# Optimization experiments

Measured on AMD Instinct MI355X. Metric: run time of the kernel, lower is better.

Reference implementation:

```python
import jax, jax.numpy as jnp
import numpy as np
from jax import lax

B, T, S, J, D = 8, 512, 32, 64, 400
R, MDU, TAGS = 256, 100, 7


def _lstm(x, Wih, Whh, bih, bhh):
    """PyTorch-convention LSTM over x [N,L,Din]; gate order i,f,g,o.
    Returns (hs, cs) each [N,L,R] in scan order (not re-flipped)."""
    N = x.shape[0]
    Rh = Whh.shape[1]
    h0 = jnp.zeros((N, Rh), x.dtype)
    xW = x @ Wih.T + (bih + bhh)  # precompute input projection [N,L,4R]

    def step(carry, xt):
        h, c = carry
        g = xt + h @ Whh.T
        i, f, gg, o = jnp.split(g, 4, axis=-1)
        c = jax.nn.sigmoid(f) * c + jax.nn.sigmoid(i) * jnp.tanh(gg)
        h = jax.nn.sigmoid(o) * jnp.tanh(c)
        return (h, c), (h, c)

    _, (hs, cs) = lax.scan(step, (h0, h0), xW.transpose(1, 0, 2))
    return hs.transpose(1, 0, 2), cs.transpose(1, 0, 2)


def setup_inputs() -> dict:
    key = jax.random.key(0)
    ks = jax.random.split(key, 40)

    def rn(i, shape, s=0.1):
        return s * jax.random.normal(ks[i], shape, jnp.float32)

    inp = {
        'input_text': rn(0, (B, T, D), 1.0),
        'input_syn': rn(1, (B, S, J, D), 1.0),
        'label': jax.random.randint(ks[2], (B, T), 0, TAGS),
        'len_context': jnp.full((B,), T, jnp.int32),
        'len_synopsis': jnp.full((B, S), J, jnp.int32),
    }
    # 6 LSTM parameter sets: context f1/b1 (in=D), synopsis f/b (in=D), modeling f/b (in=4R)
    idx = 3
    for name, din in [('f1', D), ('b1', D), ('sf', D), ('sb', D), ('mf', 4 * R), ('mb', 4 * R)]:
        inp['Wih_' + name] = rn(idx, (4 * R, din)); idx += 1
        inp['Whh_' + name] = rn(idx, (4 * R, R)); idx += 1
        inp['bih_' + name] = rn(idx, (4 * R,)); idx += 1
        inp['bhh_' + name] = rn(idx, (4 * R,)); idx += 1
    inp['W_cWh'] = rn(idx, (MDU, 2 * R)); idx += 1
    inp['W_cWu'] = rn(idx, (MDU, 2 * R)); idx += 1
    inp['W_v'] = rn(idx, (1, MDU)); idx += 1
    inp['W_sWh'] = rn(idx, (2 * R, 2 * R)); idx += 1
    inp['W_sWu'] = rn(idx, (2 * R, 2 * R)); idx += 1
    inp['W_Ws'] = rn(idx, (MDU, 2 * R)); idx += 1
    inp['W_out'] = rn(idx, (TAGS, 6 * R)); idx += 1
    inp['b_out'] = rn(idx, (TAGS,)); idx += 1
    return inp


def reference(input_text, input_syn, label, len_context, len_synopsis,
              Wih_f1, Whh_f1, bih_f1, bhh_f1,
              Wih_b1, Whh_b1, bih_b1, bhh_b1,
              Wih_sf, Whh_sf, bih_sf, bhh_sf,
              Wih_sb, Whh_sb, bih_sb, bhh_sb,
              Wih_mf, Whh_mf, bih_mf, bhh_mf,
              Wih_mb, Whh_mb, bih_mb, bhh_mb,
              W_cWh, W_cWu, W_v, W_sWh, W_sWu, W_Ws, W_out, b_out):
    B_, T_, D_ = input_text.shape
    S_, J_ = input_syn.shape[1], input_syn.shape[2]

    mask = (jnp.arange(T_)[None, :] < len_context[:, None]).astype(input_text.dtype)

    # --- representation layer: manual bi-LSTMCell; backward hiddens kept in scan order ---
    hs_f, cs_f = _lstm(input_text, Wih_f1, Whh_f1, bih_f1, bhh_f1)
    hs_b, cs_b = _lstm(input_text[:, ::-1], Wih_b1, Whh_b1, bih_b1, bhh_b1)
    H = jnp.concatenate([hs_f, hs_b], -1) * mask[..., None]   # [B,T,2R]
    m = jnp.concatenate([cs_f, cs_b], -1) * mask[..., None]   # [B,T,2R]
    x_init = jnp.zeros((B_, 1, 2 * R), input_text.dtype)
    H_full = jnp.concatenate([x_init, H], 1)                  # H_ : [B,T+1,2R]

    # --- synopsis encoder: bi-LSTM final hidden per synopsis sentence ---
    syn = input_syn.reshape(B_ * S_, J_, D_)
    sh_f, _ = _lstm(syn, Wih_sf, Whh_sf, bih_sf, bhh_sf)
    sh_b, _ = _lstm(syn[:, ::-1], Wih_sb, Whh_sb, bih_sb, bhh_sb)
    U = jnp.concatenate([sh_f[:, -1], sh_b[:, -1]], -1).reshape(B_, S_, 2 * R)

    # --- 'ff' co-attention ---
    cWh = H @ W_cWh.T                                          # [B,T,MDU]
    cWu = U @ W_cWu.T                                          # [B,S,MDU]
    z = jnp.tanh(cWh[:, :, None, :] + cWu[:, None, :, :]) @ W_v[0]  # [B,T,S]
    alpha = jax.nn.softmax(z, axis=-1)
    c = jnp.einsum('bts,bsd->btd', alpha, U)                   # [B,T,2R]

    # --- sentinel (ATT_SYN) ---
    Hprev = H_full[:, :T_]                                     # shifted: x_init, H[0..T-2]
    e = jax.nn.sigmoid(Hprev @ W_sWh.T + Hprev @ W_sWu.T)
    s = e * jnp.tanh(m)                                        # [B,T,2R]
    z_hat = jnp.tanh(s @ W_Ws.T + cWh) @ W_v[0]                # [B,T]
    alpha_hat = jax.nn.softmax(jnp.concatenate([z, z_hat[..., None]], -1), axis=-1)
    beta = alpha_hat[:, :, S_:S_ + 1]                          # [B,T,1]
    c_hat = beta * s + (1.0 - beta) * c
    G = jnp.concatenate([H, c_hat], -1)                        # [B,T,4R]

    # --- modeling bi-LSTM (standard aligned outputs) + output projection ---
    mh_f, _ = _lstm(G, Wih_mf, Whh_mf, bih_mf, bhh_mf)
    mh_b, _ = _lstm(G[:, ::-1], Wih_mb, Whh_mb, bih_mb, bhh_mb)
    M = jnp.concatenate([mh_f, mh_b[:, ::-1]], -1)             # [B,T,2R]

    logit = jnp.concatenate([G, M], -1) @ W_out.T + b_out      # [B,T,TAGS]
    return logit
```

## Files before the change

### kernel.cpp

```cpp
#include <hip/hip_runtime.h>
#include <math.h>
#include <stddef.h>


#define BB 8
#define TT 512
#define SS 32
#define JJ 64
#define DD 400
#define RR 256
#define G4 1024
#define H2 512
#define MDU_ 100
#define TAGS_ 7
#define BT (BB*TT)
#define NSEQ (BB*SS)
#define SCH 64
#define MB1 (1024*1024)

typedef __attribute__((ext_vector_type(8))) short short8;
typedef __attribute__((ext_vector_type(4))) float floatx4;
typedef __attribute__((ext_vector_type(4))) unsigned int u32x4;
typedef unsigned short u16;
typedef unsigned int u32;

__device__ __forceinline__ float us2f(u16 u) {
    unsigned int v = ((unsigned int)u) << 16;
    return __builtin_bit_cast(float, v);
}
__device__ __forceinline__ u16 f2us(float f) {
    unsigned int v = __builtin_bit_cast(unsigned int, f);
    v += 0x7FFFu + ((v >> 16) & 1u);
    return (u16)(v >> 16);
}
__device__ __forceinline__ float ldin(const void* p, long i, int bf) {
    return bf ? us2f(((const u16*)p)[i]) : ((const float*)p)[i];
}
__device__ __forceinline__ float sigm(float x) { return 1.0f / (1.0f + expf(-x)); }
__device__ __forceinline__ float sigm_f(float x) { return 1.0f / (1.0f + __expf(-x)); }
__device__ __forceinline__ float tanh_f(float x) {
    float e = __expf(-2.0f * fabsf(x));
    float t = (1.0f - e) / (1.0f + e);
    return copysignf(t, x);
}

__global__ void detect_k(const void* x, int* flag) {
    __shared__ int cnt;
    if (threadIdx.x == 0) cnt = 0;
    __syncthreads();
    u16 lo = ((const u16*)x)[threadIdx.x * 2];
    int e = (lo >> 7) & 0xFF;
    if (e >= 118 && e <= 131) atomicAdd(&cnt, 1);
    __syncthreads();
    if (threadIdx.x == 0) *flag = (cnt > 128) ? 1 : 0;
}
__global__ void castbf_k(const void* src, long off, u16* dst, long n, const int* flag) {
    long i = (long)blockIdx.x * 256 + threadIdx.x;
    if (i < n) dst[i] = (*flag) ? ((const u16*)src)[off + i] : f2us(((const float*)src)[off + i]);
}
__global__ void castf_k(const void* src, float* dst, long n, const int* flag) {
    long i = (long)blockIdx.x * 256 + threadIdx.x;
    if (i < n) dst[i] = ldin(src, i, *flag);
}
__global__ void zero_k(u32* p, long n) {
    long i = (long)blockIdx.x * 256 + threadIdx.x;
    if (i < n) p[i] = 0u;
}
__global__ void bias_sum_k(const void* bih, const void* bhh, float* out, const int* flag) {
    int i = blockIdx.x * 256 + threadIdx.x;
    if (i < G4) out[i] = ldin(bih, i, *flag) + ldin(bhh, i, *flag);
}
__global__ void wsum_k(const void* a, const void* b, u16* o, const int* flag) {
    int i = blockIdx.x * 256 + threadIdx.x;
    if (i < H2 * H2) o[i] = f2us(ldin(a, i, *flag) + ldin(b, i, *flag));
}
__global__ void whh_frag_k(const void* Whh, u16* WF, const int* flag) {
    int i = blockIdx.x * 256 + threadIdx.x;
    if (i >= 4 * 4 * 4 * 8 * 64 * 8) return;
    int j  = i & 7;
    int ln = (i >> 3) & 63;
    int c  = (i >> 9) & 7;
    int t  = (i >> 12) & 3;
    int w  = (i >> 14) & 3;
    int s  = (i >> 16) & 3;
    int n_g = w * 256 + s * 64 + t * 16 + (ln & 15);
    int k   = c * 32 + (ln >> 4) * 8 + j;
    WF[i] = f2us(ldin(Whh, (long)n_g * 256 + k, *flag));
}

#define BM 128
#define BN 128
#define BK 32
#define LDT 40

__global__ __launch_bounds__(256)
void gemm_bt(const u16* __restrict__ A, int lda,
             const u16* __restrict__ W, int ldw,
             void* __restrict__ C, int ldc,
             const float* __restrict__ bias,
             int M, int N, int K, int outBf16)
{
    __shared__ alignas(16) short As[BM * LDT];
    __shared__ alignas(16) short Bs[BN * LDT];
    const int tid  = threadIdx.x;
    const int m0   = blockIdx.y * BM;
    const int n0   = blockIdx.x * BN;
    const int lane = tid & 63;
    const int wave = tid >> 6;
    const int wm   = wave >> 1, wn = wave & 1;
    const int quad = lane >> 4, mrow = lane & 15;

    floatx4 acc[4][4];
#pragma unroll
    for (int i = 0; i < 4; ++i)
#pragma unroll
        for (int j = 0; j < 4; ++j) { floatx4 z4 = {0.f,0.f,0.f,0.f}; acc[i][j] = z4; }

    for (int k0 = 0; k0 < K; k0 += BK) {
#pragma unroll
        for (int cc = 0; cc < 2; ++cc) {
            int c   = tid + cc * 256;
            int row = c >> 2;
            int kc  = (c & 3) << 3;
            int gk  = k0 + kc;
            {
                int gr = m0 + row;
                short8 v;
                if (gr < M && gk + 8 <= K) {
                    v = *(const short8*)(A + (size_t)gr * lda + gk);
                } else {
#pragma unroll
                    for (int e = 0; e < 8; ++e)
                        v[e] = (gr < M && (gk + e) < K) ? (short)A[(size_t)gr * lda + gk + e] : (short)0;
                }
                *(short8*)&As[row * LDT + kc] = v;
            }
            {
                int gn = n0 + row;
                short8 v;
                if (gn < N && gk + 8 <= K) {
                    v = *(const short8*)(W + (size_t)gn * ldw + gk);
                } else {
#pragma unroll
                    for (int e = 0; e < 8; ++e)
                        v[e] = (gn < N && (gk + e) < K) ? (short)W[(size_t)gn * ldw + gk + e] : (short)0;
                }
                *(short8*)&Bs[row * LDT + kc] = v;
            }
        }
        __syncthreads();

        short8 af[4], bf[4];
#pragma unroll
        for (int i = 0; i < 4; ++i)
            af[i] = *(const short8*)&As[(wm * 64 + i * 16 + mrow) * LDT + quad * 8];
#pragma unroll
        for (int j = 0; j < 4; ++j)
            bf[j] = *(const short8*)&Bs[(wn * 64 + j * 16 + mrow) * LDT + quad * 8];
#pragma unroll
        for (int i = 0; i < 4; ++i)
#pragma unroll
            for (int j = 0; j < 4; ++j)
                acc[i][j] = __builtin_amdgcn_mfma_f32_16x16x32_bf16(af[i], bf[j], acc[i][j], 0, 0, 0);
        __syncthreads();
    }

#pragma unroll
    for (int i = 0; i < 4; ++i)
#pragma unroll
        for (int j = 0; j < 4; ++j)
#pragma unroll
            for (int r = 0; r < 4; ++r) {
                int row = m0 + wm * 64 + i * 16 + quad * 4 + r;
                int col = n0 + wn * 64 + j * 16 + mrow;
                if (row < M && col < N) {
                    float v = acc[i][j][r];
                    if (bias) v += bias[col];
                    if (outBf16) ((u16*)C)[(size_t)row * ldc + col] = f2us(v);
                    else         ((float*)C)[(size_t)row * ldc + col] = v;
                }
            }
}

__global__ __launch_bounds__(256, 1)
void lstm_coop(const u16* __restrict__ xWf, const u16* __restrict__ xWb,
               const u16* __restrict__ WFf, const u16* __restrict__ WFb,
               int L,
               u16* __restrict__ hOut, int hStride,
               u16* __restrict__ cOut, int cStride,
               const int* __restrict__ lenp,
               int writeAtSource, int lastOnly, int seqBase,
               u32* __restrict__ hx32, u32* __restrict__ flags, int grpBase)
{
    const int s   = blockIdx.x;
    const int dir = blockIdx.y;
    const int bat = blockIdx.z;
    const int nb  = gridDim.z;
    const int tid = threadIdx.x;
    const int wv  = tid >> 6;
    const int ln  = tid & 63;
    const int q   = ln >> 4, m = ln & 15;
    const u16* xW = dir ? xWb : xWf;
    const u16* WF = dir ? WFb : WFf;
    const int grp = grpBase + dir * nb + bat;
    u32* flg = flags + (size_t)grp * 16;
    u32* hx  = hx32 + (size_t)grp * 2048;

    __shared__ float g_s[4 * 8 * 64];
    __shared__ float c_s[8 * 64];

    short8 bw[4][8];
    {
        const u16* wb = WF + ((size_t)(s * 4 + wv) * 32) * 512 + ln * 8;
#pragma unroll
        for (int t4 = 0; t4 < 4; ++t4)
#pragma unroll
            for (int c = 0; c < 8; ++c)
                bw[t4][c] = *(const short8*)(wb + (size_t)(t4 * 8 + c) * 512);
    }
    for (int i = tid; i < 512; i += 256) c_s[i] = 0.f;
    __syncthreads();

    const int seqU = tid >> 5;
    const int j0   = (tid & 31) * 2;
    const int gcol = s * 64 + j0;
    const int mylen = lenp ? lenp[bat * 8 + seqU] : 0x7fffffff;

    u32 px0, px1, px2, px3;
    {
        const int tt0 = dir ? (L - 1) : 0;
        const u16* xr = xW + (((size_t)(bat * 8 + seqU)) * L + tt0) * G4 + gcol;
        px0 = *(const u32*)xr;
        px1 = *(const u32*)(xr + 256);
        px2 = *(const u32*)(xr + 512);
        px3 = *(const u32*)(xr + 768);
    }

    for (int t = 0; t < L; ++t) {
        const int tt = dir ? (L - 1 - t) : t;
        short8 a[8];
        if (t > 0) {
            const u32* hp = hx + ((t - 1) & 1) * 1024 + m * 128;
#pragma unroll
            for (int c = 0; c < 8; ++c) {
                if (m < 8) {
                    u32x4 v = *(const u32x4*)(hp + c * 16 + q * 4);
                    a[c] = __builtin_bit_cast(short8, v);
                } else {
                    short8 z = {0,0,0,0,0,0,0,0}; a[c] = z;
                }
            }
        } else {
            short8 z = {0,0,0,0,0,0,0,0};
#pragma unroll
            for (int c = 0; c < 8; ++c) a[c] = z;
        }
        floatx4 acc[4];
#pragma unroll
        for (int t4 = 0; t4 < 4; ++t4) { floatx4 z4 = {0.f,0.f,0.f,0.f}; acc[t4] = z4; }
#pragma unroll
        for (int c = 0; c < 8; ++c)
#pragma unroll
            for (int t4 = 0; t4 < 4; ++t4)
                acc[t4] = __builtin_amdgcn_mfma_f32_16x16x32_bf16(a[c], bw[t4][c], acc[t4], 0, 0, 0);
        if (q < 2) {
#pragma unroll
            for (int t4 = 0; t4 < 4; ++t4)
#pragma unroll
                for (int r = 0; r < 4; ++r)
                    g_s[(wv * 8 + q * 4 + r) * 64 + t4 * 16 + m] = acc[t4][r];
        }
        __syncthreads();
        float hn0, hn1, cn0, cn1;
        {
            float i0 = g_s[(0 * 8 + seqU) * 64 + j0]     + us2f((u16)(px0 & 0xffffu));
            float i1 = g_s[(0 * 8 + seqU) * 64 + j0 + 1] + us2f((u16)(px0 >> 16));
            float f0 = g_s[(1 * 8 + seqU) * 64 + j0]     + us2f((u16)(px1 & 0xffffu));
            float f1 = g_s[(1 * 8 + seqU) * 64 + j0 + 1] + us2f((u16)(px1 >> 16));
            float g0 = g_s[(2 * 8 + seqU) * 64 + j0]     + us2f((u16)(px2 & 0xffffu));
            float g1 = g_s[(2 * 8 + seqU) * 64 + j0 + 1] + us2f((u16)(px2 >> 16));
            float o0 = g_s[(3 * 8 + seqU) * 64 + j0]     + us2f((u16)(px3 & 0xffffu));
            float o1 = g_s[(3 * 8 + seqU) * 64 + j0 + 1] + us2f((u16)(px3 >> 16));
            float cA = c_s[seqU * 64 + j0], cB = c_s[seqU * 64 + j0 + 1];
            cn0 = sigm_f(f0) * cA + sigm_f(i0) * tanh_f(g0);
            cn1 = sigm_f(f1) * cB + sigm_f(i1) * tanh_f(g1);
            hn0 = sigm_f(o0) * tanh_f(cn0);
            hn1 = sigm_f(o1) * tanh_f(cn1);
            c_s[seqU * 64 + j0] = cn0;
            c_s[seqU * 64 + j0 + 1] = cn1;
            u32 hpack = (u32)f2us(hn0) | ((u32)f2us(hn1) << 16);
            __hip_atomic_store(hx + (t & 1) * 1024 + seqU * 128 + (gcol >> 1),
                               hpack, __ATOMIC_RELAXED, __HIP_MEMORY_SCOPE_AGENT);
        }
        asm volatile("s_waitcnt vmcnt(0)" ::: "memory");
        __syncthreads();
        const bool last = (t == L - 1);
        if (tid == 0 && !last)
            __hip_atomic_store(&flg[s], (u32)(t + 1),
                               __ATOMIC_RELEASE, __HIP_MEMORY_SCOPE_AGENT);
        if (!lastOnly) {
            int wr = writeAtSource ? tt : t;
            float mk = (wr >= mylen) ? 0.f : 1.f;
            size_t ro = ((size_t)(bat * 8 + seqU)) * L + wr;
            u32 hp2 = (u32)f2us(hn0 * mk) | ((u32)f2us(hn1 * mk) << 16);
            *(u32*)(hOut + ro * hStride + dir * RR + gcol) = hp2;
            if (cOut) {
                u32 cp2 = (u32)f2us(cn0 * mk) | ((u32)f2us(cn1 * mk) << 16);
                *(u32*)(cOut + ro * cStride + dir * RR + gcol) = cp2;
            }
        } else if (last) {
            size_t ro = (size_t)(seqBase + bat * 8 + seqU);
            u32 hp2 = (u32)f2us(hn0) | ((u32)f2us(hn1) << 16);
            *(u32*)(hOut + ro * hStride + dir * RR + gcol) = hp2;
        }
        if (!last) {
            {
                const int tn = dir ? (L - 2 - t) : (t + 1);
                const u16* xr = xW + (((size_t)(bat * 8 + seqU)) * L + tn) * G4 + gcol;
                px0 = *(const u32*)xr;
                px1 = *(const u32*)(xr + 256);
                px2 = *(const u32*)(xr + 512);
                px3 = *(const u32*)(xr + 768);
            }
            if (tid == 0) {
                u32 tgt = (u32)(t + 1);
                long guard = 0;
                for (;;) {
                    u32 f0 = __hip_atomic_load(&flg[0], __ATOMIC_RELAXED, __HIP_MEMORY_SCOPE_AGENT);
                    u32 f1 = __hip_atomic_load(&flg[1], __ATOMIC_RELAXED, __HIP_MEMORY_SCOPE_AGENT);
                    u32 f2 = __hip_atomic_load(&flg[2], __ATOMIC_RELAXED, __HIP_MEMORY_SCOPE_AGENT);
                    u32 f3 = __hip_atomic_load(&flg[3], __ATOMIC_RELAXED, __HIP_MEMORY_SCOPE_AGENT);
                    if (f0 >= tgt && f1 >= tgt && f2 >= tgt && f3 >= tgt) break;
                    if (++guard > (1L << 18)) break;
                    if (guard > 32) __builtin_amdgcn_s_sleep(1);
                }
                if (__hip_atomic_load(&flg[0], __ATOMIC_ACQUIRE, __HIP_MEMORY_SCOPE_AGENT)
                    == 0xFFFFFFFFu)
                    __builtin_amdgcn_s_sleep(1);
            }
            __syncthreads();
        }
    }
}

__global__ void hprev_k(const u16* __restrict__ G, u16* __restrict__ Hp) {
    int idx = blockIdx.x * 256 + threadIdx.x;
    if (idx < BT * H2) {
        int r = idx >> 9, d = idx & 511;
        int t = r & (TT - 1);
        Hp[idx] = (t == 0) ? (u16)0 : G[(size_t)(r - 1) * G4 + d];
    }
}
__global__ void s_k(const float* __restrict__ e, const u16* __restrict__ mB,
                    u16* __restrict__ sB) {
    int i = blockIdx.x * 256 + threadIdx.x;
    if (i < BT * H2) sB[i] = f2us(sigm(e[i]) * tanhf(us2f(mB[i])));
}
__global__ void z_k(const float* __restrict__ cWh, const float* __restrict__ cWu,
                    const float* __restrict__ Wv, float* __restrict__ z) {
    int idx = blockIdx.x * 256 + threadIdx.x;
    if (idx >= BT * SS) return;
    int r = idx >> 5, s = idx & 31;
    int b = r >> 9;
    const float* ph = cWh + (size_t)r * MDU_;
    const float* pu = cWu + (size_t)(b * SS + s) * MDU_;
    float acc = 0.f;
    for (int j = 0; j < MDU_; ++j) acc += tanhf(ph[j] + pu[j]) * Wv[j];
    z[idx] = acc;
}
__global__ void zhat_k(const float* __restrict__ sW, const float* __restrict__ cWh,
                       const float* __restrict__ Wv, float* __restrict__ zhat) {
    int r = blockIdx.x * 256 + threadIdx.x;
    if (r >= BT) return;
    float acc = 0.f;
    const float* ps = sW + (size_t)r * MDU_;
    const float* ph = cWh + (size_t)r * MDU_;
    for (int j = 0; j < MDU_; ++j) acc += tanhf(ps[j] + ph[j]) * Wv[j];
    zhat[r] = acc;
}
__global__ __launch_bounds__(64)
void attn_mix_k(const float* __restrict__ z, const float* __restrict__ zhat,
                const u16* __restrict__ U, const u16* __restrict__ sB,
                u16* __restrict__ G) {
    int r = blockIdx.x;
    int lane = threadIdx.x;
    int b = r >> 9;
    __shared__ float alpha[SS];
    float zv = (lane < SS) ? z[(size_t)r * SS + lane] : -1e30f;
    float mx = zv;
    for (int o = 32; o > 0; o >>= 1) mx = fmaxf(mx, __shfl_xor(mx, o));
    float ez = (lane < SS) ? expf(zv - mx) : 0.f;
    float s1 = ez;
    for (int o = 32; o > 0; o >>= 1) s1 += __shfl_xor(s1, o);
    float zh = zhat[r];
    float mx2 = fmaxf(mx, zh);
    float denom = s1 * expf(mx - mx2) + expf(zh - mx2);
    float beta = expf(zh - mx2) / denom;
    if (lane < SS) alpha[lane] = ez / s1;
    __syncthreads();
    for (int d = lane; d < H2; d += 64) {
        float cv = 0.f;
#pragma unroll 8
        for (int s2 = 0; s2 < SS; ++s2)
            cv += alpha[s2] * us2f(U[(size_t)(b * SS + s2) * H2 + d]);
        float sv = us2f(sB[(size_t)r * H2 + d]);
        G[(size_t)r * G4 + H2 + d] = f2us(beta * sv + (1.f - beta) * cv);
    }
}
__global__ __launch_bounds__(256)
void logit_k(const u16* __restrict__ G, const u16* __restrict__ Mb,
             const u16* __restrict__ Wout, const float* __restrict__ boutF,
             void* __restrict__ out, const int* __restrict__ flag) {
    int r = blockIdx.x * 4 + (threadIdx.x >> 6);
    if (r >= BT) return;
    int lane = threadIdx.x & 63;
    float acc[TAGS_] = {0, 0, 0, 0, 0, 0, 0};
    for (int k = lane; k < 1536; k += 64) {
        float v = (k < G4) ? us2f(G[(size_t)r * G4 + k]) : us2f(Mb[(size_t)r * H2 + (k - G4)]);
#pragma unroll
        for (int tg = 0; tg < TAGS_; ++tg) acc[tg] += v * us2f(Wout[tg * 1536 + k]);
    }
#pragma unroll
    for (int tg = 0; tg < TAGS_; ++tg) {
        float s = acc[tg];
        for (int o = 32; o > 0; o >>= 1) s += __shfl_xor(s, o);
        acc[tg] = s;
    }
    if (lane == 0) {
        int bf = *flag;
#pragma unroll
        for (int tg = 0; tg < TAGS_; ++tg) {
            float v = acc[tg] + boutF[tg];
            if (bf) ((u16*)out)[(size_t)r * TAGS_ + tg] = f2us(v);
            else    ((float*)out)[(size_t)r * TAGS_ + tg] = v;
        }
    }
}

extern "C" void kernel_launch(void* const* d_in, const int* in_sizes, int n_in,
                              void* d_out, int out_size, void* d_ws, size_t ws_size,
                              hipStream_t stream)
{
    const void* x_text = d_in[0];
    const void* x_syn  = d_in[1];
    const int* len_ctx = (const int*)d_in[3];
    const void *Wih[6], *Whh[6], *bih[6], *bhh[6];
    for (int l = 0; l < 6; ++l) {
        Wih[l] = d_in[5 + l * 4 + 0];
        Whh[l] = d_in[5 + l * 4 + 1];
        bih[l] = d_in[5 + l * 4 + 2];
        bhh[l] = d_in[5 + l * 4 + 3];
    }
    const void* W_cWh = d_in[29];
    const void* W_cWu = d_in[30];
    const void* W_v   = d_in[31];
    const void* W_sWh = d_in[32];
    const void* W_sWu = d_in[33];
    const void* W_Ws  = d_in[34];
    const void* W_out = d_in[35];
    const void* b_out = d_in[36];
    (void)in_sizes; (void)n_in; (void)out_size;

    char* ws = (char*)d_ws;
    size_t off = 0;
    auto alloc = [&](size_t bytes) -> void* {
        void* p = ws + off;
        off += (bytes + 255) & ~(size_t)255;
        return p;
    };
    int*   flagB  = (int*)alloc(256);
    float* bsum[6];
    for (int l = 0; l < 6; ++l) bsum[l] = (float*)alloc((size_t)G4 * 4);
    u16*   WsumB  = (u16*)alloc((size_t)H2 * H2 * 2);
    u16*   Ub     = (u16*)alloc((size_t)NSEQ * H2 * 2);
    u16*   Gb     = (u16*)alloc((size_t)BT * G4 * 2);
    u16*   mMb    = (u16*)alloc((size_t)BT * H2 * 2);
    float* cWhB   = (float*)alloc((size_t)BT * MDU_ * 4);
    float* cWuB   = (float*)alloc((size_t)NSEQ * MDU_ * 4);
    float* sWB    = (float*)alloc((size_t)BT * MDU_ * 4);
    float* zB     = (float*)alloc((size_t)BT * SS * 4);
    float* zhatB  = (float*)alloc((size_t)BT * 4);
    u16*   Wcwh16 = (u16*)alloc((size_t)MDU_ * H2 * 2);
    u16*   Wcwu16 = (u16*)alloc((size_t)MDU_ * H2 * 2);
    u16*   Wws16  = (u16*)alloc((size_t)MDU_ * H2 * 2);
    u16*   Wout16 = (u16*)alloc((size_t)TAGS_ * 1536 * 2);
    float* WvF    = (float*)alloc((size_t)MDU_ * 4);
    float* boutF  = (float*)alloc((size_t)TAGS_ * 4);
    u16*   WF[6];
    for (int l = 0; l < 6; ++l) WF[l] = (u16*)alloc((size_t)G4 * RR * 2);
    u32*   cnts   = (u32*)alloc((size_t)128 * 16 * 4);
    u32*   hx32   = (u32*)alloc((size_t)128 * 2048 * 4);

    size_t fixedEnd = off;
    bool bigws = (ws_size >= fixedEnd + (size_t)81 * MB1);
    char* BIG = (char*)alloc(bigws ? (size_t)80 * MB1 : (size_t)24 * MB1);

    u16*   bufA  = (u16*)BIG;
    u16*   bufB  = (u16*)(BIG + (size_t)8 * MB1);
    u16*   x16   = (u16*)(BIG + (size_t)16 * MB1);
    u16*   W16a  = (u16*)(BIG + (size_t)19 * MB1 + MB1 / 2);
    u16*   W16b  = (u16*)(BIG + (size_t)20 * MB1 + MB1 / 2);
    u16*   HprevB = (u16*)BIG;
    float* eBuf   = (float*)(BIG + (size_t)4 * MB1);
    u16*   sBuf   = (u16*)(BIG + (size_t)12 * MB1);
    u16*   mxWf  = (u16*)BIG;
    u16*   mxWb  = (u16*)(BIG + (size_t)8 * MB1);
    u16*   W16aD = (u16*)(BIG + (size_t)16 * MB1);
    u16*   W16bD = (u16*)(BIG + (size_t)18 * MB1);
    u16*   mbufA = (u16*)BIG;
    u16*   mbufB = (u16*)(BIG + (size_t)32 * MB1);
    u16*   mx16  = (u16*)(BIG + (size_t)64 * MB1);
    u16*   mW16a = (u16*)(BIG + (size_t)78 * MB1);
    u16*   mW16b = (u16*)(BIG + (size_t)79 * MB1);

    auto cgrid = [](long n) { return dim3((unsigned)((n + 255) / 256)); };

    detect_k<<<dim3(1), dim3(256), 0, stream>>>(x_text, flagB);
    zero_k<<<cgrid(128 * 16), dim3(256), 0, stream>>>(cnts, 128 * 16);
    castbf_k<<<cgrid(MDU_ * H2), dim3(256), 0, stream>>>(W_cWh, 0, Wcwh16, MDU_ * H2, flagB);
    castbf_k<<<cgrid(MDU_ * H2), dim3(256), 0, stream>>>(W_cWu, 0, Wcwu16, MDU_ * H2, flagB);
    castbf_k<<<cgrid(MDU_ * H2), dim3(256), 0, stream>>>(W_Ws, 0, Wws16, MDU_ * H2, flagB);
    castbf_k<<<cgrid(TAGS_ * 1536), dim3(256), 0, stream>>>(W_out, 0, Wout16, TAGS_ * 1536, flagB);
    castf_k<<<cgrid(MDU_), dim3(256), 0, stream>>>(W_v, WvF, MDU_, flagB);
    castf_k<<<cgrid(TAGS_), dim3(256), 0, stream>>>(b_out, boutF, TAGS_, flagB);
    for (int l = 0; l < 6; ++l) {
        bias_sum_k<<<dim3(4), dim3(256), 0, stream>>>(bih[l], bhh[l], bsum[l], flagB);
        whh_frag_k<<<dim3(1024), dim3(256), 0, stream>>>(Whh[l], WF[l], flagB);
    }
    wsum_k<<<cgrid(H2 * H2), dim3(256), 0, stream>>>(W_sWh, W_sWu, WsumB, flagB);

    if (bigws) {
        castbf_k<<<cgrid(G4 * DD), dim3(256), 0, stream>>>(Wih[2], 0, mW16a, G4 * DD, flagB);
        castbf_k<<<cgrid(G4 * DD), dim3(256), 0, stream>>>(Wih[3], 0, mW16b, G4 * DD, flagB);
        castbf_k<<<cgrid((long)NSEQ * JJ * DD), dim3(256), 0, stream>>>(x_syn, 0, mx16, (long)NSEQ * JJ * DD, flagB);
        gemm_bt<<<dim3(8, (NSEQ * JJ) / BM), dim3(256), 0, stream>>>(mx16, DD, mW16a, DD, mbufA, G4, bsum[2], NSEQ * JJ, G4, DD, 1);
        gemm_bt<<<dim3(8, (NSEQ * JJ) / BM), dim3(256), 0, stream>>>(mx16, DD, mW16b, DD, mbufB, G4, bsum[3], NSEQ * JJ, G4, DD, 1);
        lstm_coop<<<dim3(4, 2, 32), dim3(256), 0, stream>>>(
            mbufA, mbufB, WF[2], WF[3], JJ,
            Ub, H2, (u16*)nullptr, 0, (const int*)nullptr,
            0, 1, 0, hx32, cnts, 2);
    } else {
        castbf_k<<<cgrid(G4 * DD), dim3(256), 0, stream>>>(Wih[2], 0, W16a, G4 * DD, flagB);
        castbf_k<<<cgrid(G4 * DD), dim3(256), 0, stream>>>(Wih[3], 0, W16b, G4 * DD, flagB);
        for (int c = 0; c < NSEQ / SCH; ++c) {
            long chunkElems = (long)SCH * JJ * DD;
            castbf_k<<<cgrid(chunkElems), dim3(256), 0, stream>>>(x_syn, (long)c * chunkElems, x16, chunkElems, flagB);
            gemm_bt<<<dim3(8, (SCH * JJ) / BM), dim3(256), 0, stream>>>(x16, DD, W16a, DD, bufA, G4, bsum[2], SCH * JJ, G4, DD, 1);
            gemm_bt<<<dim3(8, (SCH * JJ) / BM), dim3(256), 0, stream>>>(x16, DD, W16b, DD, bufB, G4, bsum[3], SCH * JJ, G4, DD, 1);
            lstm_coop<<<dim3(4, 2, 8), dim3(256), 0, stream>>>(
                bufA, bufB, WF[2], WF[3], JJ,
                Ub, H2, (u16*)nullptr, 0, (const int*)nullptr,
                0, 1, c * SCH, hx32, cnts, 2 + c * 16);
        }
    }

    castbf_k<<<cgrid((long)BT * DD), dim3(256), 0, stream>>>(x_text, 0, x16, (long)BT * DD, flagB);
    castbf_k<<<cgrid(G4 * DD), dim3(256), 0, stream>>>(Wih[0], 0, W16a, G4 * DD, flagB);
    castbf_k<<<cgrid(G4 * DD), dim3(256), 0, stream>>>(Wih[1], 0, W16b, G4 * DD, flagB);
    gemm_bt<<<dim3(8, 32), dim3(256), 0, stream>>>(x16, DD, W16a, DD, bufA, G4, bsum[0], BT, G4, DD, 1);
    gemm_bt<<<dim3(8, 32), dim3(256), 0, stream>>>(x16, DD, W16b, DD, bufB, G4, bsum[1], BT, G4, DD, 1);
    lstm_coop<<<dim3(4, 2, 1), dim3(256), 0, stream>>>(
        bufA, bufB, WF[0], WF[1], TT,
        Gb, G4, mMb, H2, len_ctx, 0, 0, 0, hx32, cnts, 0);

    gemm_bt<<<dim3(1, 32), dim3(256), 0, stream>>>(Gb, G4, Wcwh16, H2, cWhB, MDU_, nullptr, BT, MDU_, H2, 0);
    gemm_bt<<<dim3(1, 2),  dim3(256), 0, stream>>>(Ub, H2, Wcwu16, H2, cWuB, MDU_, nullptr, NSEQ, MDU_, H2, 0);
    hprev_k<<<cgrid(BT * H2), dim3(256), 0, stream>>>(Gb, HprevB);
    gemm_bt<<<dim3(4, 32), dim3(256), 0, stream>>>(HprevB, H2, WsumB, H2, eBuf, H2, nullptr, BT, H2, H2, 0);
    s_k<<<cgrid(BT * H2), dim3(256), 0, stream>>>(eBuf, mMb, sBuf);
    gemm_bt<<<dim3(1, 32), dim3(256), 0, stream>>>(sBuf, H2, Wws16, H2, sWB, MDU_, nullptr, BT, MDU_, H2, 0);
    z_k<<<cgrid(BT * SS), dim3(256), 0, stream>>>(cWhB, cWuB, WvF, zB);
    zhat_k<<<cgrid(BT), dim3(256), 0, stream>>>(sWB, cWhB, WvF, zhatB);
    attn_mix_k<<<dim3(BT), dim3(64), 0, stream>>>(zB, zhatB, Ub, sBuf, Gb);

    castbf_k<<<cgrid(G4 * G4), dim3(256), 0, stream>>>(Wih[4], 0, W16aD, G4 * G4, flagB);
    castbf_k<<<cgrid(G4 * G4), dim3(256), 0, stream>>>(Wih[5], 0, W16bD, G4 * G4, flagB);
    gemm_bt<<<dim3(8, 32), dim3(256), 0, stream>>>(Gb, G4, W16aD, G4, mxWf, G4, bsum[4], BT, G4, G4, 1);
    gemm_bt<<<dim3(8, 32), dim3(256), 0, stream>>>(Gb, G4, W16bD, G4, mxWb, G4, bsum[5], BT, G4, G4, 1);
    lstm_coop<<<dim3(4, 2, 1), dim3(256), 0, stream>>>(
        mxWf, mxWb, WF[4], WF[5], TT,
        mMb, H2, (u16*)nullptr, 0, (const int*)nullptr, 1, 0, 0, hx32, cnts, 66);

    logit_k<<<dim3(BT / 4), dim3(256), 0, stream>>>(Gb, mMb, Wout16, boutF, d_out, flagB);
}
```

Before: 4.396 ms.

## Interleave forward and backward LSTM directions within each cooperative block

Each cooperative LSTM block now runs both directions, alternating forward and backward steps. It keeps both directions' recurrent weights in registers and uses separate flag and h-exchange slots per direction. The aim is to hide the cross-block spin-wait of one direction behind the other direction's MFMA and gate work, and to halve the grid. The costs are doubled weight registers (possible spills), half as many blocks running in parallel, and more serialized work per block. Group indices and the hx buffer size were adjusted to match.

```diff
diff --git a/kernel.cpp b/kernel.cpp
--- a/kernel.cpp
+++ b/kernel.cpp
@@ -193,32 +193,29 @@
                u32* __restrict__ hx32, u32* __restrict__ flags, int grpBase)
 {
     const int s   = blockIdx.x;
-    const int dir = blockIdx.y;
-    const int bat = blockIdx.z;
-    const int nb  = gridDim.z;
+    const int bat = blockIdx.y;
     const int tid = threadIdx.x;
     const int wv  = tid >> 6;
     const int ln  = tid & 63;
     const int q   = ln >> 4, m = ln & 15;
-    const u16* xW = dir ? xWb : xWf;
-    const u16* WF = dir ? WFb : WFf;
-    const int grp = grpBase + dir * nb + bat;
+    const int grp = grpBase + bat;
     u32* flg = flags + (size_t)grp * 16;
-    u32* hx  = hx32 + (size_t)grp * 2048;
+    u32* hxg = hx32 + (size_t)grp * 4096;
 
     __shared__ float g_s[4 * 8 * 64];
-    __shared__ float c_s[8 * 64];
-
-    short8 bw[4][8];
-    {
-        const u16* wb = WF + ((size_t)(s * 4 + wv) * 32) * 512 + ln * 8;
+    __shared__ float c_s[2][8 * 64];
+
+    short8 bw[2][4][8];
+#pragma unroll
+    for (int d = 0; d < 2; ++d) {
+        const u16* wb = (d ? WFb : WFf) + ((size_t)(s * 4 + wv) * 32) * 512 + ln * 8;
 #pragma unroll
         for (int t4 = 0; t4 < 4; ++t4)
 #pragma unroll
             for (int c = 0; c < 8; ++c)
-                bw[t4][c] = *(const short8*)(wb + (size_t)(t4 * 8 + c) * 512);
-    }
-    for (int i = tid; i < 512; i += 256) c_s[i] = 0.f;
+                bw[d][t4][c] = *(const short8*)(wb + (size_t)(t4 * 8 + c) * 512);
+    }
+    for (int i = tid; i < 1024; i += 256) ((float*)c_s)[i] = 0.f;
     __syncthreads();
 
     const int seqU = tid >> 5;
@@ -226,119 +223,118 @@
     const int gcol = s * 64 + j0;
     const int mylen = lenp ? lenp[bat * 8 + seqU] : 0x7fffffff;
 
-    u32 px0, px1, px2, px3;
-    {
-        const int tt0 = dir ? (L - 1) : 0;
-        const u16* xr = xW + (((size_t)(bat * 8 + seqU)) * L + tt0) * G4 + gcol;
-        px0 = *(const u32*)xr;
-        px1 = *(const u32*)(xr + 256);
-        px2 = *(const u32*)(xr + 512);
-        px3 = *(const u32*)(xr + 768);
+    u32 px[2][4];
+#pragma unroll
+    for (int d = 0; d < 2; ++d) {
+        const int tt0 = d ? (L - 1) : 0;
+        const u16* xr = (d ? xWb : xWf) + (((size_t)(bat * 8 + seqU)) * L + tt0) * G4 + gcol;
+        px[d][0] = *(const u32*)xr;
+        px[d][1] = *(const u32*)(xr + 256);
+        px[d][2] = *(const u32*)(xr + 512);
+        px[d][3] = *(const u32*)(xr + 768);
     }
 
     for (int t = 0; t < L; ++t) {
-        const int tt = dir ? (L - 1 - t) : t;
-        short8 a[8];
-        if (t > 0) {
-            const u32* hp = hx + ((t - 1) & 1) * 1024 + m * 128;
-#pragma unroll
-            for (int c = 0; c < 8; ++c) {
-                if (m < 8) {
-                    u32x4 v = *(const u32x4*)(hp + c * 16 + q * 4);
-                    a[c] = __builtin_bit_cast(short8, v);
-                } else {
-                    short8 z = {0,0,0,0,0,0,0,0}; a[c] = z;
-                }
-            }
-        } else {
-            short8 z = {0,0,0,0,0,0,0,0};
-#pragma unroll
-            for (int c = 0; c < 8; ++c) a[c] = z;
-        }
-        floatx4 acc[4];
-#pragma unroll
-        for (int t4 = 0; t4 < 4; ++t4) { floatx4 z4 = {0.f,0.f,0.f,0.f}; acc[t4] = z4; }
-#pragma unroll
-        for (int c = 0; c < 8; ++c)
-#pragma unroll
-            for (int t4 = 0; t4 < 4; ++t4)
-                acc[t4] = __builtin_amdgcn_mfma_f32_16x16x32_bf16(a[c], bw[t4][c], acc[t4], 0, 0, 0);
-        if (q < 2) {
-#pragma unroll
-            for (int t4 = 0; t4 < 4; ++t4)
-#pragma unroll
-                for (int r = 0; r < 4; ++r)
-                    g_s[(wv * 8 + q * 4 + r) * 64 + t4 * 16 + m] = acc[t4][r];
-        }
-        __syncthreads();
-        float hn0, hn1, cn0, cn1;
-        {
-            float i0 = g_s[(0 * 8 + seqU) * 64 + j0]     + us2f((u16)(px0 & 0xffffu));
-            float i1 = g_s[(0 * 8 + seqU) * 64 + j0 + 1] + us2f((u16)(px0 >> 16));
-            float f0 = g_s[(1 * 8 + seqU) * 64 + j0]     + us2f((u16)(px1 & 0xffffu));
-            float f1 = g_s[(1 * 8 + seqU) * 64 + j0 + 1] + us2f((u16)(px1 >> 16));
-            float g0 = g_s[(2 * 8 + seqU) * 64 + j0]     + us2f((u16)(px2 & 0xffffu));
-            float g1 = g_s[(2 * 8 + seqU) * 64 + j0 + 1] + us2f((u16)(px2 >> 16));
-            float o0 = g_s[(3 * 8 + seqU) * 64 + j0]     + us2f((u16)(px3 & 0xffffu));
-            float o1 = g_s[(3 * 8 + seqU) * 64 + j0 + 1] + us2f((u16)(px3 >> 16));
-            float cA = c_s[seqU * 64 + j0], cB = c_s[seqU * 64 + j0 + 1];
-            cn0 = sigm_f(f0) * cA + sigm_f(i0) * tanh_f(g0);
-            cn1 = sigm_f(f1) * cB + sigm_f(i1) * tanh_f(g1);
-            hn0 = sigm_f(o0) * tanh_f(cn0);
-            hn1 = sigm_f(o1) * tanh_f(cn1);
-            c_s[seqU * 64 + j0] = cn0;
-            c_s[seqU * 64 + j0 + 1] = cn1;
-            u32 hpack = (u32)f2us(hn0) | ((u32)f2us(hn1) << 16);
-            __hip_atomic_store(hx + (t & 1) * 1024 + seqU * 128 + (gcol >> 1),
-                               hpack, __ATOMIC_RELAXED, __HIP_MEMORY_SCOPE_AGENT);
-        }
-        asm volatile("s_waitcnt vmcnt(0)" ::: "memory");
-        __syncthreads();
         const bool last = (t == L - 1);
-        if (tid == 0 && !last)
-            __hip_atomic_store(&flg[s], (u32)(t + 1),
-                               __ATOMIC_RELEASE, __HIP_MEMORY_SCOPE_AGENT);
-        if (!lastOnly) {
-            int wr = writeAtSource ? tt : t;
-            float mk = (wr >= mylen) ? 0.f : 1.f;
-            size_t ro = ((size_t)(bat * 8 + seqU)) * L + wr;
-            u32 hp2 = (u32)f2us(hn0 * mk) | ((u32)f2us(hn1 * mk) << 16);
-            *(u32*)(hOut + ro * hStride + dir * RR + gcol) = hp2;
-            if (cOut) {
-                u32 cp2 = (u32)f2us(cn0 * mk) | ((u32)f2us(cn1 * mk) << 16);
-                *(u32*)(cOut + ro * cStride + dir * RR + gcol) = cp2;
-            }
-        } else if (last) {
-            size_t ro = (size_t)(seqBase + bat * 8 + seqU);
-            u32 hp2 = (u32)f2us(hn0) | ((u32)f2us(hn1) << 16);
-            *(u32*)(hOut + ro * hStride + dir * RR + gcol) = hp2;
-        }
-        if (!last) {
-            {
-                const int tn = dir ? (L - 2 - t) : (t + 1);
-                const u16* xr = xW + (((size_t)(bat * 8 + seqU)) * L + tn) * G4 + gcol;
-                px0 = *(const u32*)xr;
-                px1 = *(const u32*)(xr + 256);
-                px2 = *(const u32*)(xr + 512);
-                px3 = *(const u32*)(xr + 768);
-            }
-            if (tid == 0) {
-                u32 tgt = (u32)(t + 1);
+#pragma unroll
+        for (int d = 0; d < 2; ++d) {
+            const int tt = d ? (L - 1 - t) : t;
+            if (t > 0) {
+                const u32 tgt = (u32)t;
                 long guard = 0;
                 for (;;) {
-                    u32 f0 = __hip_atomic_load(&flg[0], __ATOMIC_RELAXED, __HIP_MEMORY_SCOPE_AGENT);
-                    u32 f1 = __hip_atomic_load(&flg[1], __ATOMIC_RELAXED, __HIP_MEMORY_SCOPE_AGENT);
-                    u32 f2 = __hip_atomic_load(&flg[2], __ATOMIC_RELAXED, __HIP_MEMORY_SCOPE_AGENT);
-                    u32 f3 = __hip_atomic_load(&flg[3], __ATOMIC_RELAXED, __HIP_MEMORY_SCOPE_AGENT);
+                    u32 f0 = __hip_atomic_load(&flg[d * 4 + 0], __ATOMIC_RELAXED, __HIP_MEMORY_SCOPE_AGENT);
+                    u32 f1 = __hip_atomic_load(&flg[d * 4 + 1], __ATOMIC_RELAXED, __HIP_MEMORY_SCOPE_AGENT);
+                    u32 f2 = __hip_atomic_load(&flg[d * 4 + 2], __ATOMIC_RELAXED, __HIP_MEMORY_SCOPE_AGENT);
+                    u32 f3 = __hip_atomic_load(&flg[d * 4 + 3], __ATOMIC_RELAXED, __HIP_MEMORY_SCOPE_AGENT);
                     if (f0 >= tgt && f1 >= tgt && f2 >= tgt && f3 >= tgt) break;
                     if (++guard > (1L << 18)) break;
-                    if (guard > 32) __builtin_amdgcn_s_sleep(1);
+                    if (guard > 16) __builtin_amdgcn_s_sleep(1);
                 }
-                if (__hip_atomic_load(&flg[0], __ATOMIC_ACQUIRE, __HIP_MEMORY_SCOPE_AGENT)
-                    == 0xFFFFFFFFu)
-                    __builtin_amdgcn_s_sleep(1);
+                __atomic_thread_fence(__ATOMIC_ACQUIRE);
+            }
+            short8 a[8];
+            if (t > 0) {
+                const u32* hp = hxg + d * 2048 + ((t - 1) & 1) * 1024 + m * 128;
+#pragma unroll
+                for (int c = 0; c < 8; ++c) {
+                    if (m < 8) {
+                        u32x4 v = *(const u32x4*)(hp + c * 16 + q * 4);
+                        a[c] = __builtin_bit_cast(short8, v);
+                    } else {
+                        short8 z = {0,0,0,0,0,0,0,0}; a[c] = z;
+                    }
+                }
+            } else {
+                short8 z = {0,0,0,0,0,0,0,0};
+#pragma unroll
+                for (int c = 0; c < 8; ++c) a[c] = z;
+            }
+            floatx4 acc[4];
+#pragma unroll
+            for (int t4 = 0; t4 < 4; ++t4) { floatx4 z4 = {0.f,0.f,0.f,0.f}; acc[t4] = z4; }
+#pragma unroll
+            for (int c = 0; c < 8; ++c)
+#pragma unroll
+                for (int t4 = 0; t4 < 4; ++t4)
+                    acc[t4] = __builtin_amdgcn_mfma_f32_16x16x32_bf16(a[c], bw[d][t4][c], acc[t4], 0, 0, 0);
+            if (q < 2) {
+#pragma unroll
+                for (int t4 = 0; t4 < 4; ++t4)
+#pragma unroll
+                    for (int r = 0; r < 4; ++r)
+                        g_s[(wv * 8 + q * 4 + r) * 64 + t4 * 16 + m] = acc[t4][r];
             }
             __syncthreads();
+            float hn0, hn1, cn0, cn1;
+            {
+                float i0 = g_s[(0 * 8 + seqU) * 64 + j0]     + us2f((u16)(px[d][0] & 0xffffu));
+                float i1 = g_s[(0 * 8 + seqU) * 64 + j0 + 1] + us2f((u16)(px[d][0] >> 16));
+                float f0 = g_s[(1 * 8 + seqU) * 64 + j0]     + us2f((u16)(px[d][1] & 0xffffu));
+                float f1 = g_s[(1 * 8 + seqU) * 64 + j0 + 1] + us2f((u16)(px[d][1] >> 16));
+                float g0 = g_s[(2 * 8 + seqU) * 64 + j0]     + us2f((u16)(px[d][2] & 0xffffu));
+                float g1 = g_s[(2 * 8 + seqU) * 64 + j0 + 1] + us2f((u16)(px[d][2] >> 16));
+                float o0 = g_s[(3 * 8 + seqU) * 64 + j0]     + us2f((u16)(px[d][3] & 0xffffu));
+                float o1 = g_s[(3 * 8 + seqU) * 64 + j0 + 1] + us2f((u16)(px[d][3] >> 16));
+                float cA = c_s[d][seqU * 64 + j0], cB = c_s[d][seqU * 64 + j0 + 1];
+                cn0 = sigm_f(f0) * cA + sigm_f(i0) * tanh_f(g0);
+                cn1 = sigm_f(f1) * cB + sigm_f(i1) * tanh_f(g1);
+                hn0 = sigm_f(o0) * tanh_f(cn0);
+                hn1 = sigm_f(o1) * tanh_f(cn1);
+                c_s[d][seqU * 64 + j0] = cn0;
+                c_s[d][seqU * 64 + j0 + 1] = cn1;
+                u32 hpack = (u32)f2us(hn0) | ((u32)f2us(hn1) << 16);
+                __hip_atomic_store(hxg + d * 2048 + (t & 1) * 1024 + seqU * 128 + (gcol >> 1),
+                                   hpack, __ATOMIC_RELAXED, __HIP_MEMORY_SCOPE_AGENT);
+            }
+            asm volatile("s_waitcnt vmcnt(0)" ::: "memory");
+            __syncthreads();
+            if (tid == 0 && !last)
+                __hip_atomic_store(&flg[d * 4 + s], (u32)(t + 1),
+                                   __ATOMIC_RELEASE, __HIP_MEMORY_SCOPE_AGENT);
+            if (!lastOnly) {
+                int wr = writeAtSource ? tt : t;
+                float mk = (wr >= mylen) ? 0.f : 1.f;
+                size_t ro = ((size_t)(bat * 8 + seqU)) * L + wr;
+                u32 hp2 = (u32)f2us(hn0 * mk) | ((u32)f2us(hn1 * mk) << 16);
+                *(u32*)(hOut + ro * hStride + d * RR + gcol) = hp2;
+                if (cOut) {
+                    u32 cp2 = (u32)f2us(cn0 * mk) | ((u32)f2us(cn1 * mk) << 16);
+                    *(u32*)(cOut + ro * cStride + d * RR + gcol) = cp2;
+                }
+            } else if (last) {
+                size_t ro = (size_t)(seqBase + bat * 8 + seqU);
+                u32 hp2 = (u32)f2us(hn0) | ((u32)f2us(hn1) << 16);
+                *(u32*)(hOut + ro * hStride + d * RR + gcol) = hp2;
+            }
+            if (!last) {
+                const int tn = d ? (L - 2 - t) : (t + 1);
+                const u16* xr = (d ? xWb : xWf) + (((size_t)(bat * 8 + seqU)) * L + tn) * G4 + gcol;
+                px[d][0] = *(const u32*)xr;
+                px[d][1] = *(const u32*)(xr + 256);
+                px[d][2] = *(const u32*)(xr + 512);
+                px[d][3] = *(const u32*)(xr + 768);
+            }
         }
     }
 }
@@ -489,7 +485,7 @@
     u16*   WF[6];
     for (int l = 0; l < 6; ++l) WF[l] = (u16*)alloc((size_t)G4 * RR * 2);
     u32*   cnts   = (u32*)alloc((size_t)128 * 16 * 4);
-    u32*   hx32   = (u32*)alloc((size_t)128 * 2048 * 4);
+    u32*   hx32   = (u32*)alloc((size_t)128 * 4096 * 4);
 
     size_t fixedEnd = off;
     bool bigws = (ws_size >= fixedEnd + (size_t)81 * MB1);
@@ -535,7 +531,7 @@
         castbf_k<<<cgrid((long)NSEQ * JJ * DD), dim3(256), 0, stream>>>(x_syn, 0, mx16, (long)NSEQ * JJ * DD, flagB);
         gemm_bt<<<dim3(8, (NSEQ * JJ) / BM), dim3(256), 0, stream>>>(mx16, DD, mW16a, DD, mbufA, G4, bsum[2], NSEQ * JJ, G4, DD, 1);
         gemm_bt<<<dim3(8, (NSEQ * JJ) / BM), dim3(256), 0, stream>>>(mx16, DD, mW16b, DD, mbufB, G4, bsum[3], NSEQ * JJ, G4, DD, 1);
-        lstm_coop<<<dim3(4, 2, 32), dim3(256), 0, stream>>>(
+        lstm_coop<<<dim3(4, 32), dim3(256), 0, stream>>>(
             mbufA, mbufB, WF[2], WF[3], JJ,
             Ub, H2, (u16*)nullptr, 0, (const int*)nullptr,
             0, 1, 0, hx32, cnts, 2);
@@ -547,10 +543,10 @@
             castbf_k<<<cgrid(chunkElems), dim3(256), 0, stream>>>(x_syn, (long)c * chunkElems, x16, chunkElems, flagB);
             gemm_bt<<<dim3(8, (SCH * JJ) / BM), dim3(256), 0, stream>>>(x16, DD, W16a, DD, bufA, G4, bsum[2], SCH * JJ, G4, DD, 1);
             gemm_bt<<<dim3(8, (SCH * JJ) / BM), dim3(256), 0, stream>>>(x16, DD, W16b, DD, bufB, G4, bsum[3], SCH * JJ, G4, DD, 1);
-            lstm_coop<<<dim3(4, 2, 8), dim3(256), 0, stream>>>(
+            lstm_coop<<<dim3(4, 8), dim3(256), 0, stream>>>(
                 bufA, bufB, WF[2], WF[3], JJ,
                 Ub, H2, (u16*)nullptr, 0, (const int*)nullptr,
-                0, 1, c * SCH, hx32, cnts, 2 + c * 16);
+                0, 1, c * SCH, hx32, cnts, 2 + c * 8);
         }
     }
 
@@ -559,7 +555,7 @@
     castbf_k<<<cgrid(G4 * DD), dim3(256), 0, stream>>>(Wih[1], 0, W16b, G4 * DD, flagB);
     gemm_bt<<<dim3(8, 32), dim3(256), 0, stream>>>(x16, DD, W16a, DD, bufA, G4, bsum[0], BT, G4, DD, 1);
     gemm_bt<<<dim3(8, 32), dim3(256), 0, stream>>>(x16, DD, W16b, DD, bufB, G4, bsum[1], BT, G4, DD, 1);
-    lstm_coop<<<dim3(4, 2, 1), dim3(256), 0, stream>>>(
+    lstm_coop<<<dim3(4, 1), dim3(256), 0, stream>>>(
         bufA, bufB, WF[0], WF[1], TT,
         Gb, G4, mMb, H2, len_ctx, 0, 0, 0, hx32, cnts, 0);
 
@@ -577,9 +573,9 @@
     castbf_k<<<cgrid(G4 * G4), dim3(256), 0, stream>>>(Wih[5], 0, W16bD, G4 * G4, flagB);
     gemm_bt<<<dim3(8, 32), dim3(256), 0, stream>>>(Gb, G4, W16aD, G4, mxWf, G4, bsum[4], BT, G4, G4, 1);
     gemm_bt<<<dim3(8, 32), dim3(256), 0, stream>>>(Gb, G4, W16bD, G4, mxWb, G4, bsum[5], BT, G4, G4, 1);
-    lstm_coop<<<dim3(4, 2, 1), dim3(256), 0, stream>>>(
+    lstm_coop<<<dim3(4, 1), dim3(256), 0, stream>>>(
         mxWf, mxWb, WF[4], WF[5], TT,
-        mMb, H2, (u16*)nullptr, 0, (const int*)nullptr, 1, 0, 0, hx32, cnts, 66);
+        mMb, H2, (u16*)nullptr, 0, (const int*)nullptr, 1, 0, 0, hx32, cnts, 1);
 
     logit_k<<<dim3(BT / 4), dim3(256), 0, stream>>>(Gb, mMb, Wout16, boutF, d_out, flagB);
 }
```

Result: slower. 7.859 ms (+78.8%).
